# Kernel optimization log

Measured on AMD Instinct MI355X. Metric: run time of the kernel, lower is better.

The kernel has to match this reference:

```python
import jax, jax.numpy as jnp
import numpy as np

HIGHEST_ID = 222.0
ZERO_NONZERO_PENALTY = 1.0
N_COEFFS = 447  # Chebyshev.fit(..., deg=446)


def _cheb_eval(x, coeffs):
    """Evaluate sum_i coeffs[i] * T_i(x/111 - 1) via O(1)-memory three-term recurrence."""
    xn = x / 111.0 - 1.0
    T0 = jnp.ones_like(xn)
    T1 = xn
    acc0 = coeffs[0] * T0 + coeffs[1] * T1

    def step(carry, c):
        Tm1, Tn, acc = carry
        Tnew = 2.0 * xn * Tn - Tm1
        acc = acc + c * Tnew
        return (Tn, Tnew, acc), None

    (_, _, acc), _ = jax.lax.scan(step, (T0, T1, acc0), coeffs[2:])
    return acc


def _round_ste(x):
    return x + jax.lax.stop_gradient(jnp.round(x) - x)


def _mask(x):
    # ~0 for id > 222, ~id for id <= 222
    return x * jax.nn.sigmoid(50.0 * (222.5 - x))


def setup_inputs() -> dict:
    key = jax.random.key(0)
    k0, k1, k2 = jax.random.split(key, 3)
    shape = (512, 7, 16, 64, 2)
    scale = jnp.array([222.0, 200.0], dtype=jnp.float32)  # (id, amount)
    y_pred = jax.random.uniform(k0, shape, dtype=jnp.float32) * scale
    y = jax.random.uniform(k1, shape, dtype=jnp.float32) * scale
    calories_coeffs = jax.random.normal(k2, (N_COEFFS,), dtype=jnp.float32) * 0.1
    return {"y_pred": y_pred, "y": y, "calories_coeffs": calories_coeffs}


def reference(y_pred, y, calories_coeffs):
    pred_ids = y_pred[..., 0]
    pred_amounts = y_pred[..., 1]
    true_ids = y[..., 0]
    true_amounts = y[..., 1]

    id_zero_mask = 1.0 - jnp.tanh(4.0 * pred_ids)
    amount_nonzero_mask = jnp.tanh(4.0 * pred_amounts)
    case1 = id_zero_mask * amount_nonzero_mask
    case2 = (1.0 - id_zero_mask) * (1.0 - amount_nonzero_mask)
    zeros_nonzeros_penalty = (ZERO_NONZERO_PENALTY * (case1 + case2)).sum(axis=(1, 2, 3)).mean()

    id_range_penalty = jax.nn.relu(pred_ids - HIGHEST_ID).sum(axis=(1, 2, 3)).mean()

    B = y.shape[0]
    true_amounts_f = true_amounts.reshape(B, -1)
    true_calories = _cheb_eval(true_ids, calories_coeffs).reshape(B, -1)
    calories_in_true_menu = (true_calories * true_amounts_f / 100.0).sum(axis=1) / 7.0

    pred_amounts_f = pred_amounts.reshape(y_pred.shape[0], -1)
    pred_calories = _cheb_eval(_mask(_round_ste(pred_ids)), calories_coeffs).reshape(y_pred.shape[0], -1)
    calories_in_pred_menu = (pred_calories * pred_amounts_f / 100.0).sum(axis=1) / 7.0

    calories_diff = ((calories_in_true_menu - calories_in_pred_menu) ** 2).mean()

    return zeros_nonzeros_penalty + id_range_penalty + calories_diff
```

## Files before the change

### kernel.cpp

```cpp
#include <hip/hip_runtime.h>
#include <cmath>


constexpr int NCOEF = 447;
constexpr int NTAB  = 223;
constexpr int M     = 65536;
constexpr float H_STEP = (float)(3.14159265358979323846 / 65536.0);
constexpr float SCALE  = (float)(65536.0 / 3.14159265358979323846);
constexpr int TPB = 256;
constexpr int F4_PER_HALF = 1792;

__device__ float2 g_tab[M];
__device__ float  g_pred[NTAB];
__device__ float4 g_part[1024];

__device__ __forceinline__ float tanh4(float v) {
  float e = __expf(8.0f * v);
  return fmaf(-2.0f, __builtin_amdgcn_rcpf(e + 1.0f), 1.0f);
}

__global__ __launch_bounds__(256)
void build_tables(const float* __restrict__ coeffs)
{
  int g = blockIdx.x * 256 + threadIdx.x;
  float x;
  if (g <= M) {
    x = cosf((float)g * H_STEP);
  } else if (g < M + 1 + NTAB) {
    float kf = (float)(g - (M + 1));
    float m = kf / (1.0f + __expf(50.0f * (kf - 222.5f)));
    x = m / 111.0f - 1.0f;
  } else {
    return;
  }
  float x2 = x + x;
  float Ta = 1.0f, Tb = x;
  float acc = fmaf(coeffs[1], x, coeffs[0]);
  for (int i = 2; i + 1 < NCOEF; i += 2) {
    Ta = fmaf(x2, Tb, -Ta); acc = fmaf(coeffs[i],     Ta, acc);
    Tb = fmaf(x2, Ta, -Tb); acc = fmaf(coeffs[i + 1], Tb, acc);
  }
  Ta = fmaf(x2, Tb, -Ta); acc = fmaf(coeffs[NCOEF - 1], Ta, acc);

  if (g <= M) {
    if (g < M) g_tab[g].x = acc;
    if (g > 0) g_tab[g - 1].y = acc;
  } else {
    g_pred[g - (M + 1)] = acc;
  }
}

__global__ __launch_bounds__(TPB)
void loss_main(const float4* __restrict__ yp4, const float4* __restrict__ yt4)
{
  __shared__ float spred[NTAB];
  __shared__ float sred[12];
  const int tid = threadIdx.x;

  if (tid < NTAB) spred[tid] = g_pred[tid];
  __syncthreads();

  const int b = blockIdx.x >> 1, h = blockIdx.x & 1;
  const size_t base = (size_t)b * 3584 + (size_t)h * F4_PER_HALF;

  float4 p[7], t[7];
  #pragma unroll
  for (int k = 0; k < 7; ++k) {
    p[k] = yp4[base + tid + k * TPB];
    t[k] = yt4[base + tid + k * TPB];
  }

  float fr[14], tam[14];
  float2 f2[14];
  #pragma unroll
  for (int k = 0; k < 7; ++k) {
    float xn0 = t[k].x / 111.0f - 1.0f;
    float th0 = acosf(xn0) * SCALE;
    int i0 = (int)th0; i0 = i0 > M - 1 ? M - 1 : i0;
    fr[2 * k] = th0 - (float)i0; tam[2 * k] = t[k].y;
    f2[2 * k] = g_tab[i0];

    float xn1 = t[k].z / 111.0f - 1.0f;
    float th1 = acosf(xn1) * SCALE;
    int i1 = (int)th1; i1 = i1 > M - 1 ? M - 1 : i1;
    fr[2 * k + 1] = th1 - (float)i1; tam[2 * k + 1] = t[k].w;
    f2[2 * k + 1] = g_tab[i1];
  }

  float ct = 0.0f;
  #pragma unroll
  for (int k = 0; k < 14; ++k) {
    float cal = fmaf(fr[k], f2[k].y - f2[k].x, f2[k].x);
    ct = fmaf(cal, tam[k], ct);
  }

  float pen = 0.0f, cp = 0.0f;
  #pragma unroll
  for (int k = 0; k < 7; ++k) {
    float id0 = p[k].x, am0 = p[k].y, id1 = p[k].z, am1 = p[k].w;
    float a0 = tanh4(id0), b0 = tanh4(am0);
    pen += fmaf(b0, fmaf(-2.0f, a0, 1.0f), a0) + fmaxf(id0 - 222.0f, 0.0f);
    int x0 = (int)rintf(id0); x0 = x0 < 0 ? 0 : (x0 > NTAB - 1 ? NTAB - 1 : x0);
    cp = fmaf(spred[x0], am0, cp);
    float a1 = tanh4(id1), b1 = tanh4(am1);
    pen += fmaf(b1, fmaf(-2.0f, a1, 1.0f), a1) + fmaxf(id1 - 222.0f, 0.0f);
    int x1 = (int)rintf(id1); x1 = x1 < 0 ? 0 : (x1 > NTAB - 1 ? NTAB - 1 : x1);
    cp = fmaf(spred[x1], am1, cp);
  }

  #pragma unroll
  for (int o = 32; o > 0; o >>= 1) {
    pen += __shfl_down(pen, o, 64);
    ct  += __shfl_down(ct,  o, 64);
    cp  += __shfl_down(cp,  o, 64);
  }
  const int w = tid >> 6;
  if ((tid & 63) == 0) { sred[w] = pen; sred[4 + w] = ct; sred[8 + w] = cp; }
  __syncthreads();
  if (tid == 0) {
    g_part[blockIdx.x] =
        make_float4(sred[0] + sred[1] + sred[2]  + sred[3],
                    sred[4] + sred[5] + sred[6]  + sred[7],
                    sred[8] + sred[9] + sred[10] + sred[11], 0.0f);
  }
}

__global__ __launch_bounds__(512)
void finalize(float* __restrict__ out)
{
  __shared__ float sr[8];
  int t = threadIdx.x;
  float4 u = g_part[2 * t], v = g_part[2 * t + 1];
  float pen = u.x + v.x;
  float d = ((u.y + v.y) - (u.z + v.z)) * (1.0f / 700.0f);
  float s = fmaf(d, d, pen);
  #pragma unroll
  for (int o = 32; o > 0; o >>= 1) s += __shfl_down(s, o, 64);
  if ((t & 63) == 0) sr[t >> 6] = s;
  __syncthreads();
  if (t == 0) {
    out[0] = (sr[0] + sr[1] + sr[2] + sr[3] +
              sr[4] + sr[5] + sr[6] + sr[7]) * (1.0f / 512.0f);
  }
}

extern "C" void kernel_launch(void* const* d_in, const int* in_sizes, int n_in,
                              void* d_out, int out_size, void* d_ws, size_t ws_size,
                              hipStream_t stream) {
  build_tables<<<257, 256, 0, stream>>>((const float*)d_in[2]);
  loss_main<<<1024, TPB, 0, stream>>>(
      (const float4*)d_in[0], (const float4*)d_in[1]);
  finalize<<<1, 512, 0, stream>>>((float*)d_out);
}
```

Baseline: 116.8 us.

## Shrink Chebyshev table, use quadratic interpolation, and stage it in LDS

Result: faster. 107.0 us (-8.4%).

```diff
diff --git a/kernel.cpp b/kernel.cpp
--- a/kernel.cpp
+++ b/kernel.cpp
@@ -4,14 +4,13 @@
 
 constexpr int NCOEF = 447;
 constexpr int NTAB  = 223;
-constexpr int M     = 65536;
-constexpr float H_STEP = (float)(3.14159265358979323846 / 65536.0);
-constexpr float SCALE  = (float)(65536.0 / 3.14159265358979323846);
+constexpr int MQ    = 8192;
+constexpr float SCALEQ = (float)(8192.0 / 3.14159265358979323846);
+constexpr float HQ     = (float)(3.14159265358979323846 / 8192.0);
 constexpr int TPB = 256;
-constexpr int F4_PER_HALF = 1792;
 
-__device__ float2 g_tab[M];
-__device__ float  g_pred[NTAB];
+__device__ float g_tabF[MQ + 1];
+__device__ float g_pred[NTAB];
 __device__ float4 g_part[1024];
 
 __device__ __forceinline__ float tanh4(float v) {
@@ -24,10 +23,10 @@
 {
   int g = blockIdx.x * 256 + threadIdx.x;
   float x;
-  if (g <= M) {
-    x = cosf((float)g * H_STEP);
-  } else if (g < M + 1 + NTAB) {
-    float kf = (float)(g - (M + 1));
+  if (g <= MQ) {
+    x = cosf((float)g * HQ);
+  } else if (g < MQ + 1 + NTAB) {
+    float kf = (float)(g - (MQ + 1));
     float m = kf / (1.0f + __expf(50.0f * (kf - 222.5f)));
     x = m / 111.0f - 1.0f;
   } else {
@@ -42,70 +41,70 @@
   }
   Ta = fmaf(x2, Tb, -Ta); acc = fmaf(coeffs[NCOEF - 1], Ta, acc);
 
-  if (g <= M) {
-    if (g < M) g_tab[g].x = acc;
-    if (g > 0) g_tab[g - 1].y = acc;
-  } else {
-    g_pred[g - (M + 1)] = acc;
-  }
+  if (g <= MQ) g_tabF[g] = acc;
+  else         g_pred[g - (MQ + 1)] = acc;
 }
 
 __global__ __launch_bounds__(TPB)
 void loss_main(const float4* __restrict__ yp4, const float4* __restrict__ yt4)
 {
+  __shared__ __align__(16) float sf[MQ + 1];
   __shared__ float spred[NTAB];
   __shared__ float sred[12];
   const int tid = threadIdx.x;
 
+  const float4* gt4 = (const float4*)g_tabF;
+  #pragma unroll
+  for (int k = 0; k < 8; ++k) ((float4*)sf)[tid + k * TPB] = gt4[tid + k * TPB];
+  if (tid == 0) sf[MQ] = g_tabF[MQ];
   if (tid < NTAB) spred[tid] = g_pred[tid];
   __syncthreads();
 
   const int b = blockIdx.x >> 1, h = blockIdx.x & 1;
-  const size_t base = (size_t)b * 3584 + (size_t)h * F4_PER_HALF;
+  const size_t base = (size_t)b * 3584 + (size_t)h * 1792;
 
-  float4 p[7], t[7];
+  float pen = 0.0f, cp = 0.0f, ct = 0.0f;
+
   #pragma unroll
   for (int k = 0; k < 7; ++k) {
-    p[k] = yp4[base + tid + k * TPB];
-    t[k] = yt4[base + tid + k * TPB];
-  }
+    float4 pv = yp4[base + tid + k * TPB];
+    float4 tv = yt4[base + tid + k * TPB];
 
-  float fr[14], tam[14];
-  float2 f2[14];
-  #pragma unroll
-  for (int k = 0; k < 7; ++k) {
-    float xn0 = t[k].x / 111.0f - 1.0f;
-    float th0 = acosf(xn0) * SCALE;
-    int i0 = (int)th0; i0 = i0 > M - 1 ? M - 1 : i0;
-    fr[2 * k] = th0 - (float)i0; tam[2 * k] = t[k].y;
-    f2[2 * k] = g_tab[i0];
+    float a0 = tanh4(pv.x), b0 = tanh4(pv.y);
+    pen += fmaf(b0, fmaf(-2.0f, a0, 1.0f), a0) + fmaxf(pv.x - 222.0f, 0.0f);
+    int x0 = (int)rintf(pv.x); x0 = x0 < 0 ? 0 : (x0 > NTAB - 1 ? NTAB - 1 : x0);
+    cp = fmaf(spred[x0], pv.y, cp);
+    float a1 = tanh4(pv.z), b1 = tanh4(pv.w);
+    pen += fmaf(b1, fmaf(-2.0f, a1, 1.0f), a1) + fmaxf(pv.z - 222.0f, 0.0f);
+    int x1 = (int)rintf(pv.z); x1 = x1 < 0 ? 0 : (x1 > NTAB - 1 ? NTAB - 1 : x1);
+    cp = fmaf(spred[x1], pv.w, cp);
 
-    float xn1 = t[k].z / 111.0f - 1.0f;
-    float th1 = acosf(xn1) * SCALE;
-    int i1 = (int)th1; i1 = i1 > M - 1 ? M - 1 : i1;
-    fr[2 * k + 1] = th1 - (float)i1; tam[2 * k + 1] = t[k].w;
-    f2[2 * k + 1] = g_tab[i1];
-  }
-
-  float ct = 0.0f;
-  #pragma unroll
-  for (int k = 0; k < 14; ++k) {
-    float cal = fmaf(fr[k], f2[k].y - f2[k].x, f2[k].x);
-    ct = fmaf(cal, tam[k], ct);
-  }
-
-  float pen = 0.0f, cp = 0.0f;
-  #pragma unroll
-  for (int k = 0; k < 7; ++k) {
-    float id0 = p[k].x, am0 = p[k].y, id1 = p[k].z, am1 = p[k].w;
-    float a0 = tanh4(id0), b0 = tanh4(am0);
-    pen += fmaf(b0, fmaf(-2.0f, a0, 1.0f), a0) + fmaxf(id0 - 222.0f, 0.0f);
-    int x0 = (int)rintf(id0); x0 = x0 < 0 ? 0 : (x0 > NTAB - 1 ? NTAB - 1 : x0);
-    cp = fmaf(spred[x0], am0, cp);
-    float a1 = tanh4(id1), b1 = tanh4(am1);
-    pen += fmaf(b1, fmaf(-2.0f, a1, 1.0f), a1) + fmaxf(id1 - 222.0f, 0.0f);
-    int x1 = (int)rintf(id1); x1 = x1 < 0 ? 0 : (x1 > NTAB - 1 ? NTAB - 1 : x1);
-    cp = fmaf(spred[x1], am1, cp);
+    {
+      float xn = tv.x / 111.0f - 1.0f;
+      float th = acosf(xn) * SCALEQ;
+      float ir = rintf(th);
+      ir = ir < 1.0f ? 1.0f : (ir > (float)(MQ - 1) ? (float)(MQ - 1) : ir);
+      int i = (int)ir;
+      float d = th - ir;
+      float fm = sf[i - 1], f0 = sf[i], fp = sf[i + 1];
+      float ca = 0.5f * (fp - fm);
+      float cb = fmaf(0.5f, fp + fm, -f0);
+      float cal = fmaf(d, fmaf(d, cb, ca), f0);
+      ct = fmaf(cal, tv.y, ct);
+    }
+    {
+      float xn = tv.z / 111.0f - 1.0f;
+      float th = acosf(xn) * SCALEQ;
+      float ir = rintf(th);
+      ir = ir < 1.0f ? 1.0f : (ir > (float)(MQ - 1) ? (float)(MQ - 1) : ir);
+      int i = (int)ir;
+      float d = th - ir;
+      float fm = sf[i - 1], f0 = sf[i], fp = sf[i + 1];
+      float ca = 0.5f * (fp - fm);
+      float cb = fmaf(0.5f, fp + fm, -f0);
+      float cal = fmaf(d, fmaf(d, cb, ca), f0);
+      ct = fmaf(cal, tv.w, ct);
+    }
   }
 
   #pragma unroll
@@ -147,7 +146,7 @@
 extern "C" void kernel_launch(void* const* d_in, const int* in_sizes, int n_in,
                               void* d_out, int out_size, void* d_ws, size_t ws_size,
                               hipStream_t stream) {
-  build_tables<<<257, 256, 0, stream>>>((const float*)d_in[2]);
+  build_tables<<<33, 256, 0, stream>>>((const float*)d_in[2]);
   loss_main<<<1024, TPB, 0, stream>>>(
       (const float4*)d_in[0], (const float4*)d_in[1]);
   finalize<<<1, 512, 0, stream>>>((float*)d_out);
```
